# Optimization experiments

Measured on AMD Instinct MI355X. Metric: run time of the kernel, lower is better.

Reference implementation:

```python
import jax, jax.numpy as jnp
import numpy as np

WH, WW = 7, 7
N = WH * WW
HEADS = 12
HEAD_DIM = 16
EMBED = 384
INNER = HEADS * HEAD_DIM
NW = 64
B_ = 2048
SCALE = HEAD_DIM ** -0.5


def _relative_position_index():
    ch, cw = np.meshgrid(np.arange(WH), np.arange(WW), indexing='ij')
    coords = np.stack([ch.ravel(), cw.ravel()])              # [2, N]
    rel = coords[:, :, None] - coords[:, None, :]             # [2, N, N]
    rel = rel.transpose(1, 2, 0)
    rel[:, :, 0] += WH - 1
    rel[:, :, 1] += WW - 1
    rel[:, :, 0] *= 2 * WW - 1
    return jnp.asarray(rel.sum(-1), dtype=jnp.int32)          # [N, N]


def setup_inputs() -> dict:
    key = jax.random.key(0)
    ks = jax.random.split(key, 8)
    s_in = EMBED ** -0.5
    s_inner = INNER ** -0.5
    x = jax.random.normal(ks[0], (B_, N, EMBED), jnp.float32)
    # Swin shift mask: 0 or -100 per window pair
    mbits = jax.random.bernoulli(ks[1], 0.2, (NW, N, N))
    mask = jnp.where(mbits, jnp.float32(-100.0), jnp.float32(0.0))
    return {
        'x': x,
        'mask': mask,
        'Wq': jax.random.normal(ks[2], (EMBED, INNER), jnp.float32) * s_in,
        'bq': jnp.zeros((INNER,), jnp.float32),
        'Wk': jax.random.normal(ks[3], (EMBED, INNER), jnp.float32) * s_in,
        'bk': jnp.zeros((INNER,), jnp.float32),
        'Wv': jax.random.normal(ks[4], (EMBED, INNER), jnp.float32) * s_in,
        'bv': jnp.zeros((INNER,), jnp.float32),
        'Wp': jax.random.normal(ks[5], (INNER, EMBED), jnp.float32) * s_inner,
        'bp': jnp.zeros((EMBED,), jnp.float32),
        'bias_table': jax.random.normal(ks[6], ((2 * WH - 1) * (2 * WW - 1), HEADS), jnp.float32) * 0.02,
        'rel_idx': _relative_position_index(),
    }


def reference(x, mask, Wq, bq, Wk, bk, Wv, bv, Wp, bp, bias_table, rel_idx):
    B, n, _ = x.shape
    q = (x @ Wq + bq).reshape(B, n, HEADS, HEAD_DIM)
    k = (x @ Wk + bk).reshape(B, n, HEADS, HEAD_DIM)
    v = (x @ Wv + bv).reshape(B, n, HEADS, HEAD_DIM)
    attn = jnp.einsum('bnhd,bmhd->bhnm', q * SCALE, k)        # [B, H, N, N]
    bias = bias_table[rel_idx]                                 # [N, N, H]
    attn = attn + jnp.transpose(bias, (2, 0, 1))[None]
    nW = mask.shape[0]
    attn = attn.reshape(B // nW, nW, HEADS, n, n) + mask[None, :, None]
    attn = jax.nn.softmax(attn.reshape(B, HEADS, n, n), axis=-1)
    out = jnp.einsum('bhnm,bmhd->bnhd', attn, v).reshape(B, n, INNER)
    return out @ Wp + bp
```

## Files before the change

kernel.cpp:

```cpp
#include <hip/hip_runtime.h>
#include <hip/hip_bf16.h>


typedef __attribute__((ext_vector_type(8))) short  bf8;
typedef __attribute__((ext_vector_type(4))) short  bf4;
typedef __attribute__((ext_vector_type(4))) float  f4;

#define L2E 1.4426950408889634f

union VU { unsigned u[2]; bf4 v; };

__device__ __forceinline__ short f2b(float f) {
  unsigned u = __builtin_bit_cast(unsigned, f);
  unsigned r = u + 0x7fffu + ((u >> 16) & 1u);
  return (short)(r >> 16);
}
__device__ __forceinline__ unsigned pk2(float lo, float hi) {
  unsigned short l = __builtin_bit_cast(unsigned short, __float2bfloat16(lo));
  unsigned short h = __builtin_bit_cast(unsigned short, __float2bfloat16(hi));
  return (unsigned)l | ((unsigned)h << 16);
}
__device__ __forceinline__ bf4 pkbf4(f4 v) {
  VU r; r.u[0] = pk2(v[0], v[1]); r.u[1] = pk2(v[2], v[3]);
  return r.v;
}
__device__ __forceinline__ float ex2(float x) {
#if __has_builtin(__builtin_amdgcn_exp2f)
  return __builtin_amdgcn_exp2f(x);
#else
  float r; asm("v_exp_f32 %0, %1" : "=v"(r) : "v"(x)); return r;
#endif
}
__device__ __forceinline__ f4 mfma16(bf4 a, bf4 b, f4 c) {
#if __has_builtin(__builtin_amdgcn_mfma_f32_16x16x16bf16_1k)
  return __builtin_amdgcn_mfma_f32_16x16x16bf16_1k(a, b, c, 0, 0, 0);
#else
  f4 d;
  asm("v_mfma_f32_16x16x16_bf16 %0, %1, %2, %3" : "=v"(d) : "v"(a), "v"(b), "v"(c));
  return d;
#endif
}

__global__ void wa_prep(const float* __restrict__ Wq, const float* __restrict__ Wk,
                        const float* __restrict__ Wv, const float* __restrict__ Wp,
                        const float* __restrict__ btab, const int* __restrict__ ridx,
                        const float* __restrict__ mask,
                        short* __restrict__ wt, short* __restrict__ wpt,
                        float* __restrict__ biasF, float* __restrict__ maskF) {
  int id = blockIdx.x * 256 + threadIdx.x;
  const int NWT = 576 * 384, NWP = 384 * 192, NBS = 12 * 64 * 64, NMS = 64 * 64 * 64;
  if (id < NWT) {
    int row = id / 384, k = id - row * 384;
    int kind = row / 192, cc = row - kind * 192;
    const float* W = (kind == 0) ? Wq : (kind == 1 ? Wk : Wv);
    float v = W[k * 192 + cc];
    if (kind == 0) v *= 0.25f * L2E;
    wt[id] = f2b(v);
  } else if ((id -= NWT) < NWP) {
    int n = id / 192, k = id - n * 192;
    wpt[id] = f2b(Wp[k * 384 + n]);
  } else if ((id -= NWP) < NBS) {
    int h = id >> 12, rem = id & 4095;
    int n = rem >> 6, cc = rem & 63;
    int m = (cc & 3) * 16 + (cc >> 2);
    float v;
    if (n >= 49)      v = -14427.0f;
    else if (m >= 49) v = 0.0f;
    else              v = btab[ridx[m * 49 + n] * 12 + h] * L2E;
    biasF[id] = v;
  } else if ((id -= NBS) < NMS) {
    int win = id >> 12, rem = id & 4095;
    int n = rem >> 6, cc = rem & 63;
    int m = (cc & 3) * 16 + (cc >> 2);
    maskF[id] = (m < 49 && n < 49) ? mask[win * 2401 + m * 49 + n] * L2E : 0.f;
  }
}

struct __align__(16) Smem {
  union U {
    short xs[64][392];
    struct QK { short qs[64][200]; short ks[64][200]; } qk;
  } u;
};

__global__ __launch_bounds__(256, 2)
void wa_main(const float* __restrict__ x,
             const float* __restrict__ bq, const float* __restrict__ bk,
             const float* __restrict__ bv, const float* __restrict__ bp,
             const short* __restrict__ wt, const short* __restrict__ wpt,
             const float* __restrict__ biasF, const float* __restrict__ maskF,
             float* __restrict__ out) {
  __shared__ Smem sm;
  const int tid = threadIdx.x;
  const int w   = tid >> 6;
  const int lid = tid & 63;
  const int g   = lid >> 4;
  const int c   = lid & 15;
  const int blk = blockIdx.x;
  const int mwin = (blk & 63) << 12;

  {
    const float* xw = x + (size_t)blk * 18816;
    f4 xv[18];
#pragma unroll
    for (int it = 0; it < 18; it++) {
      int i = tid + it * 256;
      xv[it] = *(const f4*)(xw + (i / 96) * 384 + (i % 96) * 4);
    }
    const int iT = tid + 18 * 256;
    f4 xt = {0.f, 0.f, 0.f, 0.f};
    if (iT < 4704) xt = *(const f4*)(xw + (iT / 96) * 384 + (iT % 96) * 4);
#pragma unroll
    for (int it = 0; it < 18; it++) {
      int i = tid + it * 256;
      *(bf4*)&sm.u.xs[i / 96][(i % 96) * 4] = pkbf4(xv[it]);
    }
    if (iT < 4704) *(bf4*)&sm.u.xs[iT / 96][(iT % 96) * 4] = pkbf4(xt);
    const bf8 zz = {0,0,0,0,0,0,0,0};
#pragma unroll
    for (int it = 0; it < 3; it++) {
      int i = tid + it * 256;
      if (i < 735) { int row = 49 + i / 49, c8 = (i % 49) * 8; *(bf8*)&sm.u.xs[row][c8] = zz; }
    }
  }
  __syncthreads();

  f4 acc[4][9];
#pragma unroll
  for (int mt = 0; mt < 4; mt++)
#pragma unroll
    for (int i = 0; i < 9; i++) acc[mt][i] = (f4){0.f, 0.f, 0.f, 0.f};
  int rowb[9];
#pragma unroll
  for (int i = 0; i < 9; i++) {
    int kind = i / 3, hh = 3 * w + i % 3;
    rowb[i] = (kind * 192 + hh * 16 + c) * 384;
  }
#pragma unroll 3
  for (int ks = 0; ks < 12; ks++) {
    const int k0 = ks * 32 + g * 8;
    bf8 a[4], b[9];
#pragma unroll
    for (int mt = 0; mt < 4; mt++) a[mt] = *(const bf8*)&sm.u.xs[mt * 16 + c][k0];
#pragma unroll
    for (int i = 0; i < 9; i++) b[i] = *(const bf8*)(wt + rowb[i] + k0);
#pragma unroll
    for (int mt = 0; mt < 4; mt++)
#pragma unroll
      for (int i = 0; i < 9; i++)
        acc[mt][i] = __builtin_amdgcn_mfma_f32_16x16x32_bf16(a[mt], b[i], acc[mt][i], 0, 0, 0);
  }
  __syncthreads();

  unsigned vpk[3][4][2];
#pragma unroll
  for (int i = 0; i < 9; i++) {
    const int kind = i / 3;
    const int col = (3 * w + i % 3) * 16 + c;
    const float bb = (kind == 0) ? (0.25f * L2E) * bq[col] : (kind == 1 ? bk[col] : bv[col]);
#pragma unroll
    for (int mt = 0; mt < 4; mt++) {
      unsigned w0 = pk2(acc[mt][i][0] + bb, acc[mt][i][1] + bb);
      unsigned w1 = pk2(acc[mt][i][2] + bb, acc[mt][i][3] + bb);
      if (kind == 2) {
        vpk[i - 6][mt][0] = w0;
        vpk[i - 6][mt][1] = w1;
      } else {
        short* dst = (kind == 0) ? &sm.u.qk.qs[0][0] : &sm.u.qk.ks[0][0];
        dst[(mt * 16 + g * 4 + 0) * 200 + col] = (short)(w0 & 0xFFFFu);
        dst[(mt * 16 + g * 4 + 1) * 200 + col] = (short)(w0 >> 16);
        dst[(mt * 16 + g * 4 + 2) * 200 + col] = (short)(w1 & 0xFFFFu);
        dst[(mt * 16 + g * 4 + 3) * 200 + col] = (short)(w1 >> 16);
      }
    }
  }
  asm volatile("" ::: "memory");

  const f4 z4 = {0.f, 0.f, 0.f, 0.f};
#pragma unroll
  for (int t = 0; t < 3; t++) {
    const int h  = 3 * w + t;
    const int hb = h * 16;
    bf4 afr[4], bfr[4];
#pragma unroll
    for (int nt = 0; nt < 4; nt++)
      afr[nt] = *(const bf4*)&sm.u.qk.ks[nt * 16 + c][hb + g * 4];
#pragma unroll
    for (int mt = 0; mt < 4; mt++)
      bfr[mt] = *(const bf4*)&sm.u.qk.qs[mt * 16 + c][hb + g * 4];
    f4 s[4][4];
#pragma unroll
    for (int nt = 0; nt < 4; nt++)
#pragma unroll
      for (int mt = 0; mt < 4; mt++)
        s[nt][mt] = mfma16(afr[nt], bfr[mt], z4);
    const float* bsH = biasF + (h << 12);
#pragma unroll
    for (int nt = 0; nt < 4; nt++)
#pragma unroll
      for (int r = 0; r < 4; r++) {
        const int n = nt * 16 + g * 4 + r;
        f4 b4 = *(const f4*)&bsH[n * 64 + c * 4];
        f4 m4 = *(const f4*)&maskF[mwin + n * 64 + c * 4];
#pragma unroll
        for (int mt = 0; mt < 4; mt++)
          s[nt][mt][r] += b4[mt] + m4[mt];
      }
    float rin[4];
#pragma unroll
    for (int mt = 0; mt < 4; mt++) {
      float mx = -3e38f;
#pragma unroll
      for (int nt = 0; nt < 4; nt++)
#pragma unroll
        for (int r = 0; r < 4; r++) mx = fmaxf(mx, s[nt][mt][r]);
      mx = fmaxf(mx, __shfl_xor(mx, 16, 64));
      mx = fmaxf(mx, __shfl_xor(mx, 32, 64));
      float sum = 0.f;
#pragma unroll
      for (int nt = 0; nt < 4; nt++)
#pragma unroll
        for (int r = 0; r < 4; r++) {
          float p = ex2(s[nt][mt][r] - mx);
          s[nt][mt][r] = p;
          sum += p;
        }
      sum += __shfl_xor(sum, 16, 64);
      sum += __shfl_xor(sum, 32, 64);
      rin[mt] = 1.f / sum;
    }
    unsigned ppk[4][4][2];
#pragma unroll
    for (int nt = 0; nt < 4; nt++)
#pragma unroll
      for (int mt = 0; mt < 4; mt++) {
        ppk[nt][mt][0] = pk2(s[nt][mt][0], s[nt][mt][1]);
        ppk[nt][mt][1] = pk2(s[nt][mt][2], s[nt][mt][3]);
      }
    f4 o[4];
#pragma unroll
    for (int mt = 0; mt < 4; mt++) o[mt] = z4;
#pragma unroll
    for (int kt = 0; kt < 4; kt++) {
      VU vu; vu.u[0] = vpk[t][kt][0]; vu.u[1] = vpk[t][kt][1];
#pragma unroll
      for (int mt = 0; mt < 4; mt++) {
        VU pu; pu.u[0] = ppk[kt][mt][0]; pu.u[1] = ppk[kt][mt][1];
        o[mt] = mfma16(vu.v, pu.v, o[mt]);
      }
    }
#pragma unroll
    for (int mt = 0; mt < 4; mt++) {
      f4 ov = o[mt] * rin[mt];
      *(bf4*)&sm.u.qk.qs[mt * 16 + c][hb + g * 4] = pkbf4(ov);
    }
    asm volatile("" ::: "memory");
  }

  bf8 wb0[6];
#pragma unroll
  for (int jt = 0; jt < 6; jt++)
    wb0[jt] = *(const bf8*)(wpt + (w * 96 + jt * 16 + c) * 192 + g * 8);
  __syncthreads();

  f4 acc3[6][4];
#pragma unroll
  for (int jt = 0; jt < 6; jt++)
#pragma unroll
    for (int mt = 0; mt < 4; mt++) acc3[jt][mt] = z4;
  {
    const int k0 = g * 8;
    bf8 ao[4];
#pragma unroll
    for (int mt = 0; mt < 4; mt++) ao[mt] = *(const bf8*)&sm.u.qk.qs[mt * 16 + c][k0];
#pragma unroll
    for (int jt = 0; jt < 6; jt++)
#pragma unroll
      for (int mt = 0; mt < 4; mt++)
        acc3[jt][mt] = __builtin_amdgcn_mfma_f32_16x16x32_bf16(wb0[jt], ao[mt], acc3[jt][mt], 0, 0, 0);
  }
#pragma unroll 2
  for (int ks3 = 1; ks3 < 6; ks3++) {
    const int k0 = ks3 * 32 + g * 8;
    bf8 ao[4], wb[6];
#pragma unroll
    for (int mt = 0; mt < 4; mt++) ao[mt] = *(const bf8*)&sm.u.qk.qs[mt * 16 + c][k0];
#pragma unroll
    for (int jt = 0; jt < 6; jt++)
      wb[jt] = *(const bf8*)(wpt + (w * 96 + jt * 16 + c) * 192 + k0);
#pragma unroll
    for (int jt = 0; jt < 6; jt++)
#pragma unroll
      for (int mt = 0; mt < 4; mt++)
        acc3[jt][mt] = __builtin_amdgcn_mfma_f32_16x16x32_bf16(wb[jt], ao[mt], acc3[jt][mt], 0, 0, 0);
  }
  float* ow = out + (size_t)blk * 18816;
#pragma unroll
  for (int jt = 0; jt < 6; jt++) {
    const int colb = w * 96 + jt * 16 + g * 4;
    const f4 bp4 = *(const f4*)&bp[colb];
#pragma unroll
    for (int mt = 0; mt < 4; mt++) {
      const int m = mt * 16 + c;
      if (m < 49) {
        f4 v = acc3[jt][mt] + bp4;
        *(f4*)&ow[m * 384 + colb] = v;
      }
    }
  }
}

extern "C" void kernel_launch(void* const* d_in, const int* in_sizes, int n_in,
                              void* d_out, int out_size, void* d_ws, size_t ws_size,
                              hipStream_t stream) {
  const float* x    = (const float*)d_in[0];
  const float* mask = (const float*)d_in[1];
  const float* Wq   = (const float*)d_in[2];
  const float* bq   = (const float*)d_in[3];
  const float* Wk   = (const float*)d_in[4];
  const float* bk   = (const float*)d_in[5];
  const float* Wv   = (const float*)d_in[6];
  const float* bv   = (const float*)d_in[7];
  const float* Wp   = (const float*)d_in[8];
  const float* bp   = (const float*)d_in[9];
  const float* btab = (const float*)d_in[10];
  const int*   ridx = (const int*)d_in[11];
  float* out = (float*)d_out;

  char* ws = (char*)d_ws;
  short* wt    = (short*)ws;
  short* wpt   = (short*)(ws + 442368);
  float* biasF = (float*)(ws + 589824);
  float* maskF = (float*)(ws + 786432);

  wa_prep<<<dim3(2368), dim3(256), 0, stream>>>(Wq, Wk, Wv, Wp, btab, ridx, mask,
                                                wt, wpt, biasF, maskF);
  wa_main<<<dim3(2048), dim3(256), 0, stream>>>(x, bq, bk, bv, bp, wt, wpt, biasF, maskF, out);
}
```

Baseline: 221.4 us.

## Split window work across 8 waves with row-half partitioning and V in LDS

Doubles the block to 512 threads. Each wave now handles three heads for half of the query rows, and the output projection is split into 48-column slices per wave. Because V is now produced across waves, it is stored transposed in a new LDS buffer instead of being kept in registers, and QKV is computed in two passes (QK, then V) to limit accumulator registers. The aim is lower per-thread register pressure and more waves per CU for latency hiding. The cost is extra LDS use and barriers, and each wave re-reads the weight tiles for its row half.

```diff
diff --git a/kernel.cpp b/kernel.cpp
--- a/kernel.cpp
+++ b/kernel.cpp
@@ -5,6 +5,7 @@
 typedef __attribute__((ext_vector_type(8))) short  bf8;
 typedef __attribute__((ext_vector_type(4))) short  bf4;
 typedef __attribute__((ext_vector_type(4))) float  f4;
+typedef __attribute__((ext_vector_type(2))) float  f2;
 
 #define L2E 1.4426950408889634f
 
@@ -81,9 +82,10 @@
     short xs[64][392];
     struct QK { short qs[64][200]; short ks[64][200]; } qk;
   } u;
+  short vts[192][68];
 };
 
-__global__ __launch_bounds__(256, 2)
+__global__ __launch_bounds__(512, 4)
 void wa_main(const float* __restrict__ x,
              const float* __restrict__ bq, const float* __restrict__ bk,
              const float* __restrict__ bv, const float* __restrict__ bp,
@@ -93,6 +95,8 @@
   __shared__ Smem sm;
   const int tid = threadIdx.x;
   const int w   = tid >> 6;
+  const int hg  = w & 3;
+  const int mh  = w >> 2;
   const int lid = tid & 63;
   const int g   = lid >> 4;
   const int c   = lid & 15;
@@ -101,119 +105,163 @@
 
   {
     const float* xw = x + (size_t)blk * 18816;
-    f4 xv[18];
-#pragma unroll
-    for (int it = 0; it < 18; it++) {
-      int i = tid + it * 256;
+    f4 xv[9];
+#pragma unroll
+    for (int it = 0; it < 9; it++) {
+      int i = tid + it * 512;
       xv[it] = *(const f4*)(xw + (i / 96) * 384 + (i % 96) * 4);
     }
-    const int iT = tid + 18 * 256;
+    const int iT = tid + 9 * 512;
     f4 xt = {0.f, 0.f, 0.f, 0.f};
     if (iT < 4704) xt = *(const f4*)(xw + (iT / 96) * 384 + (iT % 96) * 4);
 #pragma unroll
-    for (int it = 0; it < 18; it++) {
-      int i = tid + it * 256;
+    for (int it = 0; it < 9; it++) {
+      int i = tid + it * 512;
       *(bf4*)&sm.u.xs[i / 96][(i % 96) * 4] = pkbf4(xv[it]);
     }
     if (iT < 4704) *(bf4*)&sm.u.xs[iT / 96][(iT % 96) * 4] = pkbf4(xt);
     const bf8 zz = {0,0,0,0,0,0,0,0};
 #pragma unroll
-    for (int it = 0; it < 3; it++) {
-      int i = tid + it * 256;
+    for (int it = 0; it < 2; it++) {
+      int i = tid + it * 512;
       if (i < 735) { int row = 49 + i / 49, c8 = (i % 49) * 8; *(bf8*)&sm.u.xs[row][c8] = zz; }
     }
   }
   __syncthreads();
 
-  f4 acc[4][9];
-#pragma unroll
-  for (int mt = 0; mt < 4; mt++)
-#pragma unroll
-    for (int i = 0; i < 9; i++) acc[mt][i] = (f4){0.f, 0.f, 0.f, 0.f};
-  int rowb[9];
-#pragma unroll
-  for (int i = 0; i < 9; i++) {
-    int kind = i / 3, hh = 3 * w + i % 3;
-    rowb[i] = (kind * 192 + hh * 16 + c) * 384;
-  }
+  unsigned qpk[3][2][2], kpk[3][2][2];
+  {
+    f4 acc6[2][6];
+#pragma unroll
+    for (int j = 0; j < 2; j++)
+#pragma unroll
+      for (int i = 0; i < 6; i++) acc6[j][i] = (f4){0.f, 0.f, 0.f, 0.f};
+    int rqk[6];
+#pragma unroll
+    for (int i = 0; i < 6; i++)
+      rqk[i] = ((i / 3) * 192 + (3 * hg + i % 3) * 16 + c) * 384;
 #pragma unroll 3
-  for (int ks = 0; ks < 12; ks++) {
-    const int k0 = ks * 32 + g * 8;
-    bf8 a[4], b[9];
-#pragma unroll
-    for (int mt = 0; mt < 4; mt++) a[mt] = *(const bf8*)&sm.u.xs[mt * 16 + c][k0];
-#pragma unroll
-    for (int i = 0; i < 9; i++) b[i] = *(const bf8*)(wt + rowb[i] + k0);
-#pragma unroll
-    for (int mt = 0; mt < 4; mt++)
-#pragma unroll
-      for (int i = 0; i < 9; i++)
-        acc[mt][i] = __builtin_amdgcn_mfma_f32_16x16x32_bf16(a[mt], b[i], acc[mt][i], 0, 0, 0);
+    for (int ks = 0; ks < 12; ks++) {
+      const int k0 = ks * 32 + g * 8;
+      bf8 a[2], b[6];
+#pragma unroll
+      for (int j = 0; j < 2; j++) a[j] = *(const bf8*)&sm.u.xs[(2 * mh + j) * 16 + c][k0];
+#pragma unroll
+      for (int i = 0; i < 6; i++) b[i] = *(const bf8*)(wt + rqk[i] + k0);
+#pragma unroll
+      for (int j = 0; j < 2; j++)
+#pragma unroll
+        for (int i = 0; i < 6; i++)
+          acc6[j][i] = __builtin_amdgcn_mfma_f32_16x16x32_bf16(a[j], b[i], acc6[j][i], 0, 0, 0);
+    }
+#pragma unroll
+    for (int i = 0; i < 3; i++) {
+      const int col = (3 * hg + i) * 16 + c;
+      const float bqv = (0.25f * L2E) * bq[col], bkv = bk[col];
+#pragma unroll
+      for (int j = 0; j < 2; j++) {
+        qpk[i][j][0] = pk2(acc6[j][i][0] + bqv, acc6[j][i][1] + bqv);
+        qpk[i][j][1] = pk2(acc6[j][i][2] + bqv, acc6[j][i][3] + bqv);
+        kpk[i][j][0] = pk2(acc6[j][3 + i][0] + bkv, acc6[j][3 + i][1] + bkv);
+        kpk[i][j][1] = pk2(acc6[j][3 + i][2] + bkv, acc6[j][3 + i][3] + bkv);
+      }
+    }
+  }
+
+  {
+    f4 acc3v[2][3];
+#pragma unroll
+    for (int j = 0; j < 2; j++)
+#pragma unroll
+      for (int i = 0; i < 3; i++) acc3v[j][i] = (f4){0.f, 0.f, 0.f, 0.f};
+    int rv[3];
+#pragma unroll
+    for (int i = 0; i < 3; i++) rv[i] = (384 + (3 * hg + i) * 16 + c) * 384;
+#pragma unroll 3
+    for (int ks = 0; ks < 12; ks++) {
+      const int k0 = ks * 32 + g * 8;
+      bf8 a[2], b[3];
+#pragma unroll
+      for (int j = 0; j < 2; j++) a[j] = *(const bf8*)&sm.u.xs[(2 * mh + j) * 16 + c][k0];
+#pragma unroll
+      for (int i = 0; i < 3; i++) b[i] = *(const bf8*)(wt + rv[i] + k0);
+#pragma unroll
+      for (int j = 0; j < 2; j++)
+#pragma unroll
+        for (int i = 0; i < 3; i++)
+          acc3v[j][i] = __builtin_amdgcn_mfma_f32_16x16x32_bf16(a[j], b[i], acc3v[j][i], 0, 0, 0);
+    }
+#pragma unroll
+    for (int i = 0; i < 3; i++) {
+      const int col = (3 * hg + i) * 16 + c;
+      const float bvv = bv[col];
+#pragma unroll
+      for (int j = 0; j < 2; j++) {
+        VU vv;
+        vv.u[0] = pk2(acc3v[j][i][0] + bvv, acc3v[j][i][1] + bvv);
+        vv.u[1] = pk2(acc3v[j][i][2] + bvv, acc3v[j][i][3] + bvv);
+        *(bf4*)&sm.vts[col][(2 * mh + j) * 16 + g * 4] = vv.v;
+      }
+    }
   }
   __syncthreads();
 
-  unsigned vpk[3][4][2];
-#pragma unroll
-  for (int i = 0; i < 9; i++) {
-    const int kind = i / 3;
-    const int col = (3 * w + i % 3) * 16 + c;
-    const float bb = (kind == 0) ? (0.25f * L2E) * bq[col] : (kind == 1 ? bk[col] : bv[col]);
-#pragma unroll
-    for (int mt = 0; mt < 4; mt++) {
-      unsigned w0 = pk2(acc[mt][i][0] + bb, acc[mt][i][1] + bb);
-      unsigned w1 = pk2(acc[mt][i][2] + bb, acc[mt][i][3] + bb);
-      if (kind == 2) {
-        vpk[i - 6][mt][0] = w0;
-        vpk[i - 6][mt][1] = w1;
-      } else {
-        short* dst = (kind == 0) ? &sm.u.qk.qs[0][0] : &sm.u.qk.ks[0][0];
-        dst[(mt * 16 + g * 4 + 0) * 200 + col] = (short)(w0 & 0xFFFFu);
-        dst[(mt * 16 + g * 4 + 1) * 200 + col] = (short)(w0 >> 16);
-        dst[(mt * 16 + g * 4 + 2) * 200 + col] = (short)(w1 & 0xFFFFu);
-        dst[(mt * 16 + g * 4 + 3) * 200 + col] = (short)(w1 >> 16);
-      }
-    }
-  }
-  asm volatile("" ::: "memory");
+#pragma unroll
+  for (int i = 0; i < 3; i++) {
+    const int col = (3 * hg + i) * 16 + c;
+#pragma unroll
+    for (int j = 0; j < 2; j++) {
+      const int rb = (2 * mh + j) * 16 + g * 4;
+#pragma unroll
+      for (int rp = 0; rp < 2; rp++) {
+        unsigned qv = qpk[i][j][rp], kv = kpk[i][j][rp];
+        sm.u.qk.qs[rb + 2 * rp][col]     = (short)(qv & 0xFFFFu);
+        sm.u.qk.qs[rb + 2 * rp + 1][col] = (short)(qv >> 16);
+        sm.u.qk.ks[rb + 2 * rp][col]     = (short)(kv & 0xFFFFu);
+        sm.u.qk.ks[rb + 2 * rp + 1][col] = (short)(kv >> 16);
+      }
+    }
+  }
+  __syncthreads();
 
   const f4 z4 = {0.f, 0.f, 0.f, 0.f};
 #pragma unroll
   for (int t = 0; t < 3; t++) {
-    const int h  = 3 * w + t;
+    const int h  = 3 * hg + t;
     const int hb = h * 16;
-    bf4 afr[4], bfr[4];
+    bf4 afr[4], bfr[2];
 #pragma unroll
     for (int nt = 0; nt < 4; nt++)
       afr[nt] = *(const bf4*)&sm.u.qk.ks[nt * 16 + c][hb + g * 4];
 #pragma unroll
-    for (int mt = 0; mt < 4; mt++)
-      bfr[mt] = *(const bf4*)&sm.u.qk.qs[mt * 16 + c][hb + g * 4];
-    f4 s[4][4];
+    for (int j = 0; j < 2; j++)
+      bfr[j] = *(const bf4*)&sm.u.qk.qs[(2 * mh + j) * 16 + c][hb + g * 4];
+    f4 s[4][2];
 #pragma unroll
     for (int nt = 0; nt < 4; nt++)
 #pragma unroll
-      for (int mt = 0; mt < 4; mt++)
-        s[nt][mt] = mfma16(afr[nt], bfr[mt], z4);
+      for (int j = 0; j < 2; j++)
+        s[nt][j] = mfma16(afr[nt], bfr[j], z4);
     const float* bsH = biasF + (h << 12);
 #pragma unroll
     for (int nt = 0; nt < 4; nt++)
 #pragma unroll
       for (int r = 0; r < 4; r++) {
-        const int n = nt * 16 + g * 4 + r;
-        f4 b4 = *(const f4*)&bsH[n * 64 + c * 4];
-        f4 m4 = *(const f4*)&maskF[mwin + n * 64 + c * 4];
-#pragma unroll
-        for (int mt = 0; mt < 4; mt++)
-          s[nt][mt][r] += b4[mt] + m4[mt];
-      }
-    float rin[4];
-#pragma unroll
-    for (int mt = 0; mt < 4; mt++) {
+        const int n  = nt * 16 + g * 4 + r;
+        const int o8 = n * 64 + c * 4 + 2 * mh;
+        f2 b2 = *(const f2*)&bsH[o8];
+        f2 m2 = *(const f2*)&maskF[mwin + o8];
+        s[nt][0][r] += b2[0] + m2[0];
+        s[nt][1][r] += b2[1] + m2[1];
+      }
+    float rin[2];
+#pragma unroll
+    for (int j = 0; j < 2; j++) {
       float mx = -3e38f;
 #pragma unroll
       for (int nt = 0; nt < 4; nt++)
 #pragma unroll
-        for (int r = 0; r < 4; r++) mx = fmaxf(mx, s[nt][mt][r]);
+        for (int r = 0; r < 4; r++) mx = fmaxf(mx, s[nt][j][r]);
       mx = fmaxf(mx, __shfl_xor(mx, 16, 64));
       mx = fmaxf(mx, __shfl_xor(mx, 32, 64));
       float sum = 0.f;
@@ -221,83 +269,67 @@
       for (int nt = 0; nt < 4; nt++)
 #pragma unroll
         for (int r = 0; r < 4; r++) {
-          float p = ex2(s[nt][mt][r] - mx);
-          s[nt][mt][r] = p;
+          float p = ex2(s[nt][j][r] - mx);
+          s[nt][j][r] = p;
           sum += p;
         }
       sum += __shfl_xor(sum, 16, 64);
       sum += __shfl_xor(sum, 32, 64);
-      rin[mt] = 1.f / sum;
-    }
-    unsigned ppk[4][4][2];
+      rin[j] = 1.f / sum;
+    }
+    unsigned ppk[4][2][2];
 #pragma unroll
     for (int nt = 0; nt < 4; nt++)
 #pragma unroll
-      for (int mt = 0; mt < 4; mt++) {
-        ppk[nt][mt][0] = pk2(s[nt][mt][0], s[nt][mt][1]);
-        ppk[nt][mt][1] = pk2(s[nt][mt][2], s[nt][mt][3]);
-      }
-    f4 o[4];
-#pragma unroll
-    for (int mt = 0; mt < 4; mt++) o[mt] = z4;
+      for (int j = 0; j < 2; j++) {
+        ppk[nt][j][0] = pk2(s[nt][j][0], s[nt][j][1]);
+        ppk[nt][j][1] = pk2(s[nt][j][2], s[nt][j][3]);
+      }
+    f4 o[2];
+#pragma unroll
+    for (int j = 0; j < 2; j++) o[j] = z4;
 #pragma unroll
     for (int kt = 0; kt < 4; kt++) {
-      VU vu; vu.u[0] = vpk[t][kt][0]; vu.u[1] = vpk[t][kt][1];
-#pragma unroll
-      for (int mt = 0; mt < 4; mt++) {
-        VU pu; pu.u[0] = ppk[kt][mt][0]; pu.u[1] = ppk[kt][mt][1];
-        o[mt] = mfma16(vu.v, pu.v, o[mt]);
-      }
-    }
-#pragma unroll
-    for (int mt = 0; mt < 4; mt++) {
-      f4 ov = o[mt] * rin[mt];
-      *(bf4*)&sm.u.qk.qs[mt * 16 + c][hb + g * 4] = pkbf4(ov);
+      bf4 va = *(const bf4*)&sm.vts[hb + c][kt * 16 + g * 4];
+#pragma unroll
+      for (int j = 0; j < 2; j++) {
+        VU pu; pu.u[0] = ppk[kt][j][0]; pu.u[1] = ppk[kt][j][1];
+        o[j] = mfma16(va, pu.v, o[j]);
+      }
+    }
+#pragma unroll
+    for (int j = 0; j < 2; j++) {
+      f4 ov = o[j] * rin[j];
+      *(bf4*)&sm.u.qk.qs[(2 * mh + j) * 16 + c][hb + g * 4] = pkbf4(ov);
     }
     asm volatile("" ::: "memory");
   }
-
-  bf8 wb0[6];
-#pragma unroll
-  for (int jt = 0; jt < 6; jt++)
-    wb0[jt] = *(const bf8*)(wpt + (w * 96 + jt * 16 + c) * 192 + g * 8);
   __syncthreads();
 
-  f4 acc3[6][4];
-#pragma unroll
-  for (int jt = 0; jt < 6; jt++)
+  f4 acc3[3][4];
+#pragma unroll
+  for (int jt = 0; jt < 3; jt++)
 #pragma unroll
     for (int mt = 0; mt < 4; mt++) acc3[jt][mt] = z4;
-  {
-    const int k0 = g * 8;
-    bf8 ao[4];
+#pragma unroll 2
+  for (int ks3 = 0; ks3 < 6; ks3++) {
+    const int k0 = ks3 * 32 + g * 8;
+    bf8 ao[4], wb[3];
 #pragma unroll
     for (int mt = 0; mt < 4; mt++) ao[mt] = *(const bf8*)&sm.u.qk.qs[mt * 16 + c][k0];
 #pragma unroll
-    for (int jt = 0; jt < 6; jt++)
-#pragma unroll
-      for (int mt = 0; mt < 4; mt++)
-        acc3[jt][mt] = __builtin_amdgcn_mfma_f32_16x16x32_bf16(wb0[jt], ao[mt], acc3[jt][mt], 0, 0, 0);
-  }
-#pragma unroll 2
-  for (int ks3 = 1; ks3 < 6; ks3++) {
-    const int k0 = ks3 * 32 + g * 8;
-    bf8 ao[4], wb[6];
-#pragma unroll
-    for (int mt = 0; mt < 4; mt++) ao[mt] = *(const bf8*)&sm.u.qk.qs[mt * 16 + c][k0];
-#pragma unroll
-    for (int jt = 0; jt < 6; jt++)
-      wb[jt] = *(const bf8*)(wpt + (w * 96 + jt * 16 + c) * 192 + k0);
-#pragma unroll
-    for (int jt = 0; jt < 6; jt++)
+    for (int jt = 0; jt < 3; jt++)
+      wb[jt] = *(const bf8*)(wpt + (w * 48 + jt * 16 + c) * 192 + k0);
+#pragma unroll
+    for (int jt = 0; jt < 3; jt++)
 #pragma unroll
       for (int mt = 0; mt < 4; mt++)
         acc3[jt][mt] = __builtin_amdgcn_mfma_f32_16x16x32_bf16(wb[jt], ao[mt], acc3[jt][mt], 0, 0, 0);
   }
   float* ow = out + (size_t)blk * 18816;
 #pragma unroll
-  for (int jt = 0; jt < 6; jt++) {
-    const int colb = w * 96 + jt * 16 + g * 4;
+  for (int jt = 0; jt < 3; jt++) {
+    const int colb = w * 48 + jt * 16 + g * 4;
     const f4 bp4 = *(const f4*)&bp[colb];
 #pragma unroll
     for (int mt = 0; mt < 4; mt++) {
@@ -335,5 +367,5 @@
 
   wa_prep<<<dim3(2368), dim3(256), 0, stream>>>(Wq, Wk, Wv, Wp, btab, ridx, mask,
                                                 wt, wpt, biasF, maskF);
-  wa_main<<<dim3(2048), dim3(256), 0, stream>>>(x, bq, bk, bv, bp, wt, wpt, biasF, maskF, out);
-}
+  wa_main<<<dim3(2048), dim3(512), 0, stream>>>(x, bq, bk, bv, bp, wt, wpt, biasF, maskF, out);
+}
```

New measurement: 327.9 us. 1.48x slower.
